# Performance work log

Measured on AMD Instinct MI355X. Metric: run time of the kernel, lower is better.

The kernel has to match this reference:

```python
import jax, jax.numpy as jnp
import numpy as np

PAD_ID, SOS_ID, EOS_ID = 0, 1, 2


def setup_inputs() -> dict:
    key = jax.random.key(0)
    ks = jax.random.split(key, 8)
    V, E, H, B = 16000, 256, 512, 8
    s = 0.05  # weight scale to keep softmax well-conditioned
    return {
        "hidden": jax.random.normal(ks[0], (1, B, H), dtype=jnp.float32),
        "embedding": jax.random.normal(ks[1], (V, E), dtype=jnp.float32) * s,
        "w_ih": jax.random.normal(ks[2], (3 * H, E), dtype=jnp.float32) * s,
        "w_hh": jax.random.normal(ks[3], (3 * H, H), dtype=jnp.float32) * s,
        "b_ih": jax.random.normal(ks[4], (3 * H,), dtype=jnp.float32) * s,
        "b_hh": jax.random.normal(ks[5], (3 * H,), dtype=jnp.float32) * s,
        "w_out": jax.random.normal(ks[6], (V, H), dtype=jnp.float32) * s,
        "b_out": jax.random.normal(ks[7], (V,), dtype=jnp.float32) * s,
        "lenseq": 12,
        "k": 5,
    }


def reference(hidden, embedding, w_ih, w_hh, b_ih, b_hh, w_out, b_out, lenseq, k):
    V, E = embedding.shape
    _, B, H = hidden.shape
    dt = hidden.dtype
    pad_onehot = jax.nn.one_hot(PAD_ID, V, dtype=dt)

    def gru_cell(x_emb, h):  # x_emb: (k,B,E), h: (k,B,H); torch nn.GRU gate order r,z,n
        gi = x_emb @ w_ih.T + b_ih
        gh = h @ w_hh.T + b_hh
        i_r, i_z, i_n = jnp.split(gi, 3, axis=-1)
        h_r, h_z, h_n = jnp.split(gh, 3, axis=-1)
        r = jax.nn.sigmoid(i_r + h_r)
        z = jax.nn.sigmoid(i_z + h_z)
        n = jnp.tanh(i_n + r * h_n)
        return (1.0 - z) * n + z * h

    def step(carry, i):
        x, h, prob, res, _ = carry
        done = (x == EOS_ID) | (x == PAD_ID)            # (k,B)
        emb = embedding[x]                               # (k,B,E)
        h_new = gru_cell(emb, h)                         # (k,B,H)
        probs = jax.nn.softmax(h_new @ w_out.T + b_out, axis=-1)  # (k,B,V)
        pred = jnp.where(done[..., None], pad_onehot, probs)
        h = jnp.where(done[..., None], h, h_new)
        res = res.at[:, i].set(pred)                     # store raw pred (pre prob-scaling), as torch.cat copies
        scores = pred * prob[..., None]                  # (k,B,V); prob stays all-ones, faithful to source
        flat = scores.transpose(1, 0, 2).reshape(B, k * V)  # beam-major flatten per batch elem
        _, idx = jax.lax.top_k(flat, k)                  # (B,k)
        beam = (idx // V).T                              # (k,B)
        tok = (idx % V).T                                # (k,B)
        res = jnp.take_along_axis(res, beam[:, None, :, None], axis=0)
        prob = jnp.take_along_axis(prob, beam, axis=0)
        h = jnp.take_along_axis(h, beam[..., None], axis=0)
        return (tok, h, prob, res, pred), None

    x0 = jnp.full((k, B), SOS_ID, dtype=jnp.int32)
    h0 = jnp.broadcast_to(hidden[0], (k, B, H))
    prob0 = jnp.ones((k, B), dtype=dt)
    res0 = jnp.zeros((k, lenseq, B, V), dtype=dt)
    pred0 = jnp.zeros((k, B, V), dtype=dt)

    (x, h, prob, res, pred), _ = jax.lax.scan(step, (x0, h0, prob0, res0, pred0), jnp.arange(lenseq))

    # final top-1 selection per batch element over (k*V) flat scores
    scores = pred * prob[..., None]
    flat = scores.transpose(1, 0, 2).reshape(B, k * V)
    best_beam = jnp.argmax(flat, axis=-1) // V           # (B,)
    out = jnp.take_along_axis(res, best_beam[None, None, :, None], axis=0)[0]  # (lenseq,B,V)
    return out
```

## Files before the change

### kernel.cpp

```cpp
#include <hip/hip_runtime.h>

#define V 16000
#define E 256
#define H 512
#define HP 516
#define BB 8
#define T 12
#define NB 250
#define NBS 256
#define TPB 1024
#define CPB 64
#define AGENT __HIP_MEMORY_SCOPE_AGENT

typedef float vfloat4 __attribute__((ext_vector_type(4)));


constexpr int W_FL   = CPB * 512;
constexpr int SH_OFF = W_FL;
constexpr int SP_OFF = SH_OFF + BB * HP;
constexpr int RS_OFF = SP_OFF + 64 * 48;
constexpr int RV_OFF = RS_OFF + 128;
constexpr int RI_OFF = RV_OFF + 128;
constexpr int SS_OFF = RI_OFF + 128;
constexpr int XN_OFF = SS_OFF + 8;
constexpr int X_OFF  = XN_OFF + 8;
constexpr int SMEM_FL = X_OFF + 8;
constexpr size_t SMEM_BYTES = (size_t)SMEM_FL * 4;

__device__ __forceinline__ float dot4(float4 a, float4 b) {
    return a.x * b.x + a.y * b.y + a.z * b.z + a.w * b.w;
}

__global__ __launch_bounds__(256) void kinit(const float* __restrict__ hidden,
                                             float* __restrict__ hA,
                                             int* __restrict__ leaf,
                                             int* __restrict__ epoch) {
    int idx = blockIdx.x * 256 + threadIdx.x;
    if (idx < BB * H) hA[idx] = hidden[idx];
    if (idx < 64 * 16) leaf[idx] = 0;
    if (idx == 0) epoch[0] = 0;
}

__device__ __forceinline__ void gridbar(int* __restrict__ leaf,
                                        int* __restrict__ epoch, int ep) {
    __syncthreads();
    if (threadIdx.x == 0) {
        int g = blockIdx.x >> 2;
        __hip_atomic_fetch_add(&leaf[g * 16], 1, __ATOMIC_RELEASE, AGENT);
    }
    if (blockIdx.x == 0) {
        if (threadIdx.x < 63) {
            int expct = (threadIdx.x == 62) ? 2 : 4;
            while (__hip_atomic_load(&leaf[threadIdx.x * 16],
                                     __ATOMIC_RELAXED, AGENT) < expct * ep)
                __builtin_amdgcn_s_sleep(1);
        }
        __syncthreads();
        if (threadIdx.x == 0)
            __hip_atomic_store(epoch, ep, __ATOMIC_RELAXED, AGENT);
    } else {
        if (threadIdx.x == 0) {
            while (__hip_atomic_load(epoch, __ATOMIC_RELAXED, AGENT) < ep)
                __builtin_amdgcn_s_sleep(1);
        }
    }
    __builtin_amdgcn_fence(__ATOMIC_ACQUIRE, "workgroup");
    __syncthreads();
}

__global__ __launch_bounds__(TPB, 4) void kmain(
    const float* __restrict__ emb_tab,
    const float* __restrict__ w_ih,
    const float* __restrict__ w_hh,
    const float* __restrict__ b_ih,
    const float* __restrict__ b_hh,
    const float* __restrict__ w_out,
    const float* __restrict__ b_out,
    float* __restrict__ hA,
    float* __restrict__ hB,
    float* __restrict__ psum,
    float* __restrict__ pval,
    int* __restrict__ pidx,
    int* __restrict__ leaf,
    int* __restrict__ epoch,
    float* __restrict__ out)
{
    extern __shared__ float smem[];
    float* w_lds  = smem;
    float* s_h    = smem + SH_OFF;
    float* s_part = smem + SP_OFF;
    float* s_e    = smem + SP_OFF;
    float* s_rsum = smem + RS_OFF;
    float* s_rval = smem + RV_OFF;
    int*   s_ridx = (int*)(smem + RI_OFF);
    float* s_S    = smem + SS_OFF;
    int*   s_Xn   = (int*)(smem + XN_OFF);
    int*   s_X    = (int*)(smem + X_OFF);

    const int blk = blockIdx.x, tid = threadIdx.x;

    for (int i = tid; i < CPB * 128; i += TPB) {
        int col = i >> 7;
        int q4  = (i & 127) << 2;
        int vv  = blk * CPB + col;
        float4 w4 = *(const float4*)(w_out + (size_t)vv * H + q4);
        int sw = q4 ^ ((col & 7) << 2) ^ (((q4 >> 5) & 7) << 2);
        *(float4*)(w_lds + col * 512 + sw) = w4;
    }
    if (tid < BB) s_X[tid] = 1;
    __syncthreads();

    const int lane = tid & 63;
    const int wv   = tid >> 6;
    const int rh   = lane & 3;
    const int kq   = (lane >> 2) & 15;
    const int rowhalf = wv & 1;
    const int cs   = wv >> 1;
    const int r    = rowhalf * 4 + rh;
    const int xw   = (cs ^ (kq & 7)) << 2;
    const int hswz = (kq & 7) << 2;

    float bo[8];
#pragma unroll
    for (int p = 0; p < 8; p++) bo[p] = b_out[blk * CPB + p * 8 + cs];

    for (int t = 0; t < T; t++) {
        const float* h_cur = (t & 1) ? hB : hA;
        float*       h_nxt = (t & 1) ? hA : hB;
        const int par = t & 1;

        if (blk < 64) {
            int hr = tid >> 7, k4 = (tid & 127) << 2;
            const unsigned long long* p =
                (const unsigned long long*)(h_cur + hr * H + k4);
            union { unsigned long long u; float f[2]; } c0, c1;
            c0.u = __hip_atomic_load(p,     __ATOMIC_RELAXED, AGENT);
            c1.u = __hip_atomic_load(p + 1, __ATOMIC_RELAXED, AGENT);
            *(float4*)(s_h + hr * HP + k4) =
                make_float4(c0.f[0], c0.f[1], c1.f[0], c1.f[1]);
        }
        __syncthreads();
        if (blk < 64 && tid < 512) {
            const int jl = tid >> 6;
            const int ar = (tid >> 3) & 7;
            const int kq8 = tid & 7;
            const int j  = blk * 8 + jl;
            const int pair = jl * 8 + ar;
            float gir = 0.f, giz = 0.f, gin = 0.f, ghr = 0.f, ghz = 0.f, ghn = 0.f;
            {
                const float* erow = emb_tab + (size_t)s_X[ar] * E;
                const float* w0 = w_ih + (size_t)j * E;
                const float* w1 = w0 + (size_t)H * E;
                const float* w2 = w1 + (size_t)H * E;
                const int k0 = kq8 * (E / 8);
                for (int k = 0; k < E / 8; k += 4) {
                    float4 ev = *(const float4*)(erow + k0 + k);
                    gir += dot4(*(const float4*)(w0 + k0 + k), ev);
                    giz += dot4(*(const float4*)(w1 + k0 + k), ev);
                    gin += dot4(*(const float4*)(w2 + k0 + k), ev);
                }
            }
            {
                const float* hrow = s_h + ar * HP;
                const float* w0 = w_hh + (size_t)j * H;
                const float* w1 = w0 + (size_t)H * H;
                const float* w2 = w1 + (size_t)H * H;
                const int k0 = kq8 * (H / 8);
                for (int k = 0; k < H / 8; k += 4) {
                    float4 hv = *(const float4*)(hrow + k0 + k);
                    ghr += dot4(*(const float4*)(w0 + k0 + k), hv);
                    ghz += dot4(*(const float4*)(w1 + k0 + k), hv);
                    ghn += dot4(*(const float4*)(w2 + k0 + k), hv);
                }
            }
            float* sp = s_part + pair * 48;
            sp[0 * 8 + kq8] = gir; sp[1 * 8 + kq8] = giz; sp[2 * 8 + kq8] = gin;
            sp[3 * 8 + kq8] = ghr; sp[4 * 8 + kq8] = ghz; sp[5 * 8 + kq8] = ghn;
        }
        __syncthreads();
        if (blk < 64 && tid < 512 && (tid & 7) == 0) {
            const int pair = (tid >> 6) * 8 + ((tid >> 3) & 7);
            const int jl = pair >> 3, ar = pair & 7;
            const int j  = blk * 8 + jl;
            const float* sp2 = s_part + pair * 48;
            float G[6];
#pragma unroll
            for (int gg = 0; gg < 6; gg++) {
                float s = 0.f;
#pragma unroll
                for (int q = 0; q < 8; q++) s += sp2[gg * 8 + q];
                G[gg] = s;
            }
            float ir  = G[0] + b_ih[j],         hr_ = G[3] + b_hh[j];
            float iz  = G[1] + b_ih[H + j],     hz  = G[4] + b_hh[H + j];
            float inn = G[2] + b_ih[2 * H + j], hn  = G[5] + b_hh[2 * H + j];
            float rg = 1.f / (1.f + __expf(-(ir + hr_)));
            float zg = 1.f / (1.f + __expf(-(iz + hz)));
            float ng = tanhf(inn + rg * hn);
            float ho = s_h[ar * HP + j];
            int xr = s_X[ar];
            bool dn = (xr == 0) || (xr == 2);
            float hv = dn ? ho : ((1.f - zg) * ng + zg * ho);
            __hip_atomic_store(&h_nxt[ar * H + j], hv, __ATOMIC_RELAXED, AGENT);
        }
        gridbar(leaf, epoch, 2 * t + 1);

        {
            int hr = tid >> 7, k4 = (tid & 127) << 2;
            const unsigned long long* p =
                (const unsigned long long*)(h_nxt + hr * H + k4);
            union { unsigned long long u; float f[2]; } c0, c1;
            c0.u = __hip_atomic_load(p,     __ATOMIC_RELAXED, AGENT);
            c1.u = __hip_atomic_load(p + 1, __ATOMIC_RELAXED, AGENT);
            int sw = k4 ^ (((k4 >> 5) & 7) << 2);
            *(float4*)(s_h + hr * HP + sw) =
                make_float4(c0.f[0], c0.f[1], c1.f[0], c1.f[1]);
        }
        __syncthreads();
        {
            float4 hreg[8];
            const float* hb = s_h + r * HP + kq * 32;
#pragma unroll
            for (int i = 0; i < 8; i++)
                hreg[i] = *(const float4*)(hb + ((4 * i) ^ hswz));

            float s_acc = 0.f, bv = -1.f; int bi = 0x7fffffff;
#pragma unroll
            for (int p = 0; p < 8; p++) {
                const int col = p * 8 + cs;
                const int vv  = blk * CPB + col;
                const float* wb = w_lds + col * 512 + kq * 32;
                float acc = 0.f;
#pragma unroll
                for (int i = 0; i < 8; i++) {
                    float4 w4 = *(const float4*)(wb + ((4 * i) ^ xw));
                    acc += dot4(w4, hreg[i]);
                }
                acc += __shfl_xor(acc, 4, 64);
                acc += __shfl_xor(acc, 8, 64);
                acc += __shfl_xor(acc, 16, 64);
                acc += __shfl_xor(acc, 32, 64);
                float ee = __expf(acc + bo[p]);
                if (kq == 0) s_e[r * 65 + col] = ee;
                s_acc += ee;
                if (ee > bv) { bv = ee; bi = vv; }
            }
            if (kq == 0) {
                s_rsum[wv * 8 + r] = s_acc;
                s_rval[wv * 8 + r] = bv;
                s_ridx[wv * 8 + r] = bi;
            } else if (kq == 1) {
                int ro = (1 - rowhalf) * 4 + rh;
                s_rsum[wv * 8 + ro] = 0.f;
                s_rval[wv * 8 + ro] = -1.f;
                s_ridx[wv * 8 + ro] = 0x7fffffff;
            }
        }
        __syncthreads();
        if (tid < 64) {
            float s  = s_rsum[tid] + s_rsum[tid + 64];
            float av = s_rval[tid], bv2 = s_rval[tid + 64];
            int   ai = s_ridx[tid], bi2 = s_ridx[tid + 64];
            float bv = av; int bi = ai;
            if (bv2 > bv || (bv2 == bv && bi2 < bi)) { bv = bv2; bi = bi2; }
#pragma unroll
            for (int m = 8; m <= 32; m <<= 1) {
                s += __shfl_xor(s, m, 64);
                float ov = __shfl_xor(bv, m, 64);
                int   oi = __shfl_xor(bi, m, 64);
                if (ov > bv || (ov == bv && oi < bi)) { bv = ov; bi = oi; }
            }
            if (tid < 8) {
                int o = (par * 8 + tid) * NBS + blk;
                __hip_atomic_store(&psum[o], s,  __ATOMIC_RELAXED, AGENT);
                __hip_atomic_store(&pval[o], bv, __ATOMIC_RELAXED, AGENT);
                __hip_atomic_store(&pidx[o], bi, __ATOMIC_RELAXED, AGENT);
            }
        }
        gridbar(leaf, epoch, 2 * t + 2);

        if (wv < 8) {
            const int base = (par * 8 + wv) * NBS;
            float s = 0.f, bv = -1.f; int bi = 0x7fffffff;
#pragma unroll
            for (int c = 0; c < 4; c++) {
                int idx = lane + 64 * c;
                if (idx < NB) {
                    int o = base + idx;
                    s += __hip_atomic_load(&psum[o], __ATOMIC_RELAXED, AGENT);
                    float ov = __hip_atomic_load(&pval[o], __ATOMIC_RELAXED, AGENT);
                    int   oi = __hip_atomic_load(&pidx[o], __ATOMIC_RELAXED, AGENT);
                    if (ov > bv || (ov == bv && oi < bi)) { bv = ov; bi = oi; }
                }
            }
            for (int m = 1; m < 64; m <<= 1) {
                s += __shfl_xor(s, m, 64);
                float ov = __shfl_xor(bv, m, 64);
                int   oi = __shfl_xor(bi, m, 64);
                if (ov > bv || (ov == bv && oi < bi)) { bv = ov; bi = oi; }
            }
            if (lane == 0) { s_S[wv] = s; s_Xn[wv] = bi; }
        }
        __syncthreads();
        {
            float* out_t = out + (size_t)t * BB * V;
            if (tid < 128) {
                int row = tid >> 4;
                int c4  = (tid & 15) << 2;
                int xr = s_X[row];
                bool dn = (xr == 0) || (xr == 2);
                float inv = 1.f / s_S[row];
                int vbase = blk * CPB + c4;
                vfloat4 o4;
                o4.x = dn ? ((vbase + 0 == 0) ? 1.f : 0.f) : s_e[row * 65 + c4 + 0] * inv;
                o4.y = dn ? ((vbase + 1 == 0) ? 1.f : 0.f) : s_e[row * 65 + c4 + 1] * inv;
                o4.z = dn ? ((vbase + 2 == 0) ? 1.f : 0.f) : s_e[row * 65 + c4 + 2] * inv;
                o4.w = dn ? ((vbase + 3 == 0) ? 1.f : 0.f) : s_e[row * 65 + c4 + 3] * inv;
                __builtin_nontemporal_store(o4,
                    (vfloat4*)(out_t + (size_t)row * V + vbase));
            }
        }
        __syncthreads();
        if (tid < 8) {
            int xo = s_X[tid];
            s_X[tid] = ((xo == 0) || (xo == 2)) ? 0 : s_Xn[tid];
        }
        __syncthreads();
    }
}

extern "C" void kernel_launch(void* const* d_in, const int* in_sizes, int n_in,
                              void* d_out, int out_size, void* d_ws, size_t ws_size,
                              hipStream_t stream) {
    (void)in_sizes; (void)n_in; (void)out_size; (void)ws_size;
    const float* hidden    = (const float*)d_in[0];
    const float* embedding = (const float*)d_in[1];
    const float* w_ih      = (const float*)d_in[2];
    const float* w_hh      = (const float*)d_in[3];
    const float* b_ih      = (const float*)d_in[4];
    const float* b_hh      = (const float*)d_in[5];
    const float* w_out     = (const float*)d_in[6];
    const float* b_out     = (const float*)d_in[7];
    float* out = (float*)d_out;

    float* ws    = (float*)d_ws;
    float* hA    = ws;
    float* hB    = hA + BB * H;
    float* psum  = hB + BB * H;
    float* pval  = psum + 2 * 8 * NBS;
    int*   pidx  = (int*)(pval + 2 * 8 * NBS);
    int*   leaf  = pidx + 2 * 8 * NBS;
    int*   epoch = leaf + 64 * 16;

    hipFuncSetAttribute((const void*)kmain,
        hipFuncAttributeMaxDynamicSharedMemorySize,
        (int)SMEM_BYTES);

    kinit<<<16, 256, 0, stream>>>(hidden, hA, leaf, epoch);
    kmain<<<NB, TPB, SMEM_BYTES, stream>>>(embedding, w_ih, w_hh, b_ih, b_hh,
                                           w_out, b_out, hA, hB, psum, pval,
                                           pidx, leaf, epoch, out);
}
```

Before: 576.7 us.

## Replace tree grid barrier with flat all-spin counter barriers

```diff
diff --git a/kernel.cpp b/kernel.cpp
--- a/kernel.cpp
+++ b/kernel.cpp
@@ -33,36 +33,38 @@
 
 __global__ __launch_bounds__(256) void kinit(const float* __restrict__ hidden,
                                              float* __restrict__ hA,
-                                             int* __restrict__ leaf,
+                                             int* __restrict__ cnt,
                                              int* __restrict__ epoch) {
     int idx = blockIdx.x * 256 + threadIdx.x;
     if (idx < BB * H) hA[idx] = hidden[idx];
-    if (idx < 64 * 16) leaf[idx] = 0;
+    if (idx < 64 * 16) cnt[idx] = 0;
     if (idx == 0) epoch[0] = 0;
 }
 
-__device__ __forceinline__ void gridbar(int* __restrict__ leaf,
-                                        int* __restrict__ epoch, int ep) {
-    __syncthreads();
-    if (threadIdx.x == 0) {
-        int g = blockIdx.x >> 2;
-        __hip_atomic_fetch_add(&leaf[g * 16], 1, __ATOMIC_RELEASE, AGENT);
+__device__ __forceinline__ void barA(int* __restrict__ cnt, int ep) {
+    __syncthreads();
+    if (blockIdx.x < 64 && threadIdx.x == 0)
+        __hip_atomic_fetch_add(&cnt[(8 + (blockIdx.x & 1)) * 16], 1,
+                               __ATOMIC_RELEASE, AGENT);
+    if (threadIdx.x < 2) {
+        while (__hip_atomic_load(&cnt[(8 + threadIdx.x) * 16],
+                                 __ATOMIC_RELAXED, AGENT) < 32 * ep)
+            __builtin_amdgcn_s_sleep(2);
     }
-    if (blockIdx.x == 0) {
-        if (threadIdx.x < 63) {
-            int expct = (threadIdx.x == 62) ? 2 : 4;
-            while (__hip_atomic_load(&leaf[threadIdx.x * 16],
-                                     __ATOMIC_RELAXED, AGENT) < expct * ep)
-                __builtin_amdgcn_s_sleep(1);
-        }
-        __syncthreads();
-        if (threadIdx.x == 0)
-            __hip_atomic_store(epoch, ep, __ATOMIC_RELAXED, AGENT);
-    } else {
-        if (threadIdx.x == 0) {
-            while (__hip_atomic_load(epoch, __ATOMIC_RELAXED, AGENT) < ep)
-                __builtin_amdgcn_s_sleep(1);
-        }
+    __builtin_amdgcn_fence(__ATOMIC_ACQUIRE, "workgroup");
+    __syncthreads();
+}
+
+__device__ __forceinline__ void barB(int* __restrict__ cnt, int ep) {
+    __syncthreads();
+    if (threadIdx.x == 0)
+        __hip_atomic_fetch_add(&cnt[(blockIdx.x & 7) * 16], 1,
+                               __ATOMIC_RELEASE, AGENT);
+    if (threadIdx.x < 8) {
+        int q = (threadIdx.x < 2) ? 32 : 31;
+        while (__hip_atomic_load(&cnt[threadIdx.x * 16],
+                                 __ATOMIC_RELAXED, AGENT) < q * ep)
+            __builtin_amdgcn_s_sleep(2);
     }
     __builtin_amdgcn_fence(__ATOMIC_ACQUIRE, "workgroup");
     __syncthreads();
@@ -81,7 +83,7 @@
     float* __restrict__ psum,
     float* __restrict__ pval,
     int* __restrict__ pidx,
-    int* __restrict__ leaf,
+    int* __restrict__ cnt,
     int* __restrict__ epoch,
     float* __restrict__ out)
 {
@@ -98,6 +100,7 @@
     int*   s_X    = (int*)(smem + X_OFF);
 
     const int blk = blockIdx.x, tid = threadIdx.x;
+    (void)epoch;
 
     for (int i = tid; i < CPB * 128; i += TPB) {
         int col = i >> 7;
@@ -203,7 +206,7 @@
             float hv = dn ? ho : ((1.f - zg) * ng + zg * ho);
             __hip_atomic_store(&h_nxt[ar * H + j], hv, __ATOMIC_RELAXED, AGENT);
         }
-        gridbar(leaf, epoch, 2 * t + 1);
+        barA(cnt, t + 1);
 
         {
             int hr = tid >> 7, k4 = (tid & 127) << 2;
@@ -277,7 +280,7 @@
                 __hip_atomic_store(&pidx[o], bi, __ATOMIC_RELAXED, AGENT);
             }
         }
-        gridbar(leaf, epoch, 2 * t + 2);
+        barB(cnt, t + 1);
 
         if (wv < 8) {
             const int base = (par * 8 + wv) * NBS;
@@ -316,8 +319,7 @@
                 o4.y = dn ? ((vbase + 1 == 0) ? 1.f : 0.f) : s_e[row * 65 + c4 + 1] * inv;
                 o4.z = dn ? ((vbase + 2 == 0) ? 1.f : 0.f) : s_e[row * 65 + c4 + 2] * inv;
                 o4.w = dn ? ((vbase + 3 == 0) ? 1.f : 0.f) : s_e[row * 65 + c4 + 3] * inv;
-                __builtin_nontemporal_store(o4,
-                    (vfloat4*)(out_t + (size_t)row * V + vbase));
+                *(vfloat4*)(out_t + (size_t)row * V + vbase) = o4;
             }
         }
         __syncthreads();
@@ -349,15 +351,15 @@
     float* psum  = hB + BB * H;
     float* pval  = psum + 2 * 8 * NBS;
     int*   pidx  = (int*)(pval + 2 * 8 * NBS);
-    int*   leaf  = pidx + 2 * 8 * NBS;
-    int*   epoch = leaf + 64 * 16;
+    int*   cnt   = pidx + 2 * 8 * NBS;
+    int*   epoch = cnt + 64 * 16;
 
     hipFuncSetAttribute((const void*)kmain,
         hipFuncAttributeMaxDynamicSharedMemorySize,
         (int)SMEM_BYTES);
 
-    kinit<<<16, 256, 0, stream>>>(hidden, hA, leaf, epoch);
+    kinit<<<16, 256, 0, stream>>>(hidden, hA, cnt, epoch);
     kmain<<<NB, TPB, SMEM_BYTES, stream>>>(embedding, w_ih, w_hh, b_ih, b_hh,
                                            w_out, b_out, hA, hB, psum, pval,
-                                           pidx, leaf, epoch, out);
-}
+                                           pidx, cnt, epoch, out);
+}
```

New measurement: 646.2 us. +12.1%, slower.
